# Kernel optimization log

Measured on AMD Instinct MI355X. Metric: run time of the kernel, lower is better.

Reference implementation:

```python
import jax, jax.numpy as jnp
import numpy as np

N, E, D, ED, H = 50000, 640000, 128, 64, 128
EPS = 1e-5


def _bn(x, gamma, beta):
    # BatchNorm1d in training mode: batch stats over rows, biased variance
    mean = jnp.mean(x, axis=0)
    var = jnp.mean(jnp.square(x - mean), axis=0)
    return (x - mean) * jax.lax.rsqrt(var + EPS) * gamma + beta


def setup_inputs() -> dict:
    key = jax.random.key(0)
    ks = jax.random.split(key, 12)

    def lin(k, fan_in, fan_out):
        return jax.random.normal(k, (fan_in, fan_out), jnp.float32) / np.sqrt(fan_in)

    return {
        "h": jax.random.normal(ks[0], (N, D), jnp.float32),
        "edge_attr": jax.random.normal(ks[1], (E, ED), jnp.float32),
        # msg MLP: Linear(2D+ED->H), BN(H), ReLU, Linear(H->H)
        "W1": lin(ks[2], 2 * D + ED, H), "b1": jnp.zeros((H,), jnp.float32),
        "g1": jnp.ones((H,), jnp.float32), "be1": jnp.zeros((H,), jnp.float32),
        "W2": lin(ks[3], H, H), "b2": jnp.zeros((H,), jnp.float32),
        # upd MLP: Linear(D+H->H), BN(H), ReLU, Linear(H->D)
        "W3": lin(ks[4], D + H, H), "b3": jnp.zeros((H,), jnp.float32),
        "g2": jnp.ones((H,), jnp.float32), "be2": jnp.zeros((H,), jnp.float32),
        "W4": lin(ks[5], H, D), "b4": jnp.zeros((D,), jnp.float32),
        # residual LayerNorm
        "ln_g": jnp.ones((D,), jnp.float32), "ln_b": jnp.zeros((D,), jnp.float32),
        "edge_index": jax.random.randint(ks[6], (2, E), 0, N, jnp.int32),
        "num_nodes": N,
    }


def reference(h, edge_attr, W1, b1, g1, be1, W2, b2, W3, b3, g2, be2, W4, b4,
              ln_g, ln_b, edge_index, num_nodes):
    src, dst = edge_index[0], edge_index[1]
    # messages: MLP_msg(h_src || h_dst || e)  -> [E, H]
    msg_in = jnp.concatenate([h[src], h[dst], edge_attr], axis=-1)  # [E, 2D+ED]
    x = _bn(msg_in @ W1 + b1, g1, be1)
    messages = jax.nn.relu(x) @ W2 + b2
    # scatter-sum aggregate into dst nodes -> [N, H]
    agg = jax.ops.segment_sum(messages, dst, num_segments=num_nodes)
    # update: MLP_upd(h || agg) -> [N, D]
    u = jnp.concatenate([h, agg], axis=-1)
    y = _bn(u @ W3 + b3, g2, be2)
    h_new = jax.nn.relu(y) @ W4 + b4
    # residual + LayerNorm
    z = h + h_new
    mu = jnp.mean(z, axis=-1, keepdims=True)
    var = jnp.mean(jnp.square(z - mu), axis=-1, keepdims=True)
    return (z - mu) * jax.lax.rsqrt(var + EPS) * ln_g + ln_b
```

## Files before the change

kernel.cpp:

```cpp
#include <hip/hip_runtime.h>
#include <hip/hip_bf16.h>

#define EPS 1e-5f
#define DIMH 128
#define K1 320
#define K3 256

typedef __attribute__((ext_vector_type(8))) short bf16x8;
typedef __attribute__((ext_vector_type(4))) short bf16x4;
typedef __attribute__((ext_vector_type(4))) float f32x4;

#define MFMA(a, b, c) __builtin_amdgcn_mfma_f32_16x16x32_bf16(a, b, c, 0, 0, 0)

static __device__ __forceinline__ unsigned short f2bf(float f) {
    union { float f; unsigned u; } v; v.f = f;
    unsigned r = v.u + 0x7FFF + ((v.u >> 16) & 1);
    return (unsigned short)(r >> 16);
}

__global__ void k_prep_w(const float* __restrict__ W1, const float* __restrict__ W3,
                         const float* __restrict__ W4,
                         unsigned short* __restrict__ W1t, unsigned short* __restrict__ W3c,
                         unsigned short* __restrict__ W4t) {
    int t = blockIdx.x * 256 + threadIdx.x;
    if (t < K1 * 128) { int k = t / 128, n = t % 128; W1t[n * K1 + k] = f2bf(W1[t]); }
    if (t < 128 * 128) {
        int k = t / 128, n = t % 128;
        W4t[n * 128 + k] = f2bf(W4[t]);
        W3c[n * K3 + k] = f2bf(W3[t]);
    }
}

__global__ void k_hb(const float* __restrict__ h, unsigned short* __restrict__ hb, int total8) {
    int t = blockIdx.x * 256 + threadIdx.x;
    if (t < total8) {
        float4 a = *(const float4*)(h + (size_t)t * 8);
        float4 b = *(const float4*)(h + (size_t)t * 8 + 4);
        union { bf16x8 v; unsigned short s[8]; } u;
        u.s[0] = f2bf(a.x); u.s[1] = f2bf(a.y); u.s[2] = f2bf(a.z); u.s[3] = f2bf(a.w);
        u.s[4] = f2bf(b.x); u.s[5] = f2bf(b.y); u.s[6] = f2bf(b.z); u.s[7] = f2bf(b.w);
        *(bf16x8*)(hb + (size_t)t * 8) = u.v;
    }
}

__global__ void k_w23(const float* __restrict__ W2, const float* __restrict__ W3,
                      unsigned short* __restrict__ W3c) {
    int t = blockIdx.x * 256 + threadIdx.x;
    int j = t & 127, i = t >> 7;
    float s = 0.f;
    for (int k = 0; k < 128; ++k) s += W2[i * 128 + k] * W3[(128 + k) * 128 + j];
    W3c[j * K3 + 128 + i] = f2bf(s);
}

__global__ void k_cvec(const float* __restrict__ b2, const float* __restrict__ W3,
                       float* __restrict__ cvec) {
    int j = threadIdx.x;
    float s = 0.f;
    for (int k = 0; k < 128; ++k) s += b2[k] * W3[(128 + k) * 128 + j];
    cvec[j] = s;
}

__global__ void k_bn(const float* __restrict__ stats, const float* __restrict__ g,
                     const float* __restrict__ be, float* __restrict__ st, float cnt) {
    int c = threadIdx.x;
    float mean = stats[c] / cnt;
    float var = stats[128 + c] / cnt - mean * mean;
    float s = g[c] * rsqrtf(var + EPS);
    st[c] = s;
    st[128 + c] = be[c] - mean * s;
}

__global__ void k_deg(const int* __restrict__ dst, int* __restrict__ deg, int E) {
    int e = blockIdx.x * 256 + threadIdx.x;
    if (e < E) atomicAdd(&deg[dst[e]], 1);
}

__global__ void k_scan(const int* __restrict__ deg, int* __restrict__ offs,
                       int* __restrict__ cursor, int NN) {
    __shared__ int ps[1024];
    int t = threadIdx.x;
    int chunk = (NN + 1023) >> 10;
    int c0 = t * chunk;
    int s = 0;
    for (int i = 0; i < chunk; ++i) { int id = c0 + i; if (id < NN) s += deg[id]; }
    ps[t] = s; __syncthreads();
    for (int off = 1; off < 1024; off <<= 1) {
        int v = (t >= off) ? ps[t - off] : 0;
        __syncthreads();
        ps[t] += v;
        __syncthreads();
    }
    int run = t ? ps[t - 1] : 0;
    for (int i = 0; i < chunk; ++i) {
        int id = c0 + i;
        if (id < NN) { cursor[id] = run; run += deg[id]; offs[id] = run; }
    }
}

__global__ void k_scatter(const int* __restrict__ dst, int* __restrict__ cursor,
                          int* __restrict__ elist, int E) {
    int e = blockIdx.x * 256 + threadIdx.x;
    if (e < E) {
        int pos = atomicAdd(&cursor[dst[e]], 1);
        elist[pos] = e;
    }
}

__global__ __launch_bounds__(256, 4) void k_msg1(
    const unsigned short* __restrict__ hb, const float* __restrict__ ea,
    const int* __restrict__ src, const int* __restrict__ dst,
    const unsigned short* __restrict__ W1t, const float* __restrict__ b1,
    unsigned short* __restrict__ xout, float* __restrict__ stats) {
    __shared__ unsigned short A[64 * K1];
    int tid = threadIdx.x, lane = tid & 63, w = tid >> 6;
    long e0 = (long)blockIdx.x * 64;

    bf16x8 bfr[10][2];
    {
        int n = (w << 5) + (lane & 15), kb = (lane >> 4) << 3;
#pragma unroll
        for (int nt = 0; nt < 2; ++nt) {
            const unsigned short* p = W1t + (size_t)(n + nt * 16) * K1 + kb;
#pragma unroll
            for (int ks = 0; ks < 10; ++ks) bfr[ks][nt] = *(const bf16x8*)(p + ks * 32);
        }
    }
    {
        int c16 = tid & 15, r2 = tid >> 4;
#pragma unroll
        for (int rr = 0; rr < 4; ++rr) {
            int row = rr * 16 + r2;
            long e = e0 + row;
            int s = src[e], d = dst[e];
            bf16x8 vs = *(const bf16x8*)(hb + (size_t)s * DIMH + c16 * 8);
            bf16x8 vd = *(const bf16x8*)(hb + (size_t)d * DIMH + c16 * 8);
            float4 ve = *(const float4*)(ea + (size_t)e * 64 + c16 * 4);
            int base = row * K1, sw = (row & 7) << 3;
            *(bf16x8*)&A[(base + c16 * 8) ^ sw] = vs;
            *(bf16x8*)&A[(base + 128 + c16 * 8) ^ sw] = vd;
            union { bf16x4 v4; unsigned short s4[4]; } u;
            u.s4[0] = f2bf(ve.x); u.s4[1] = f2bf(ve.y); u.s4[2] = f2bf(ve.z); u.s4[3] = f2bf(ve.w);
            *(bf16x4*)&A[(base + 256 + c16 * 4) ^ sw] = u.v4;
        }
    }
    __syncthreads();

    f32x4 acc[4][2] = {};
#pragma unroll
    for (int rg = 0; rg < 4; ++rg) {
        int arow = rg * 16 + (lane & 15);
        int base = arow * K1, sw = (arow & 7) << 3, kb = (lane >> 4) << 3;
#pragma unroll
        for (int ks = 0; ks < 10; ++ks) {
            bf16x8 af = *(const bf16x8*)&A[(base + ks * 32 + kb) ^ sw];
            acc[rg][0] = MFMA(af, bfr[ks][0], acc[rg][0]);
            acc[rg][1] = MFMA(af, bfr[ks][1], acc[rg][1]);
        }
    }
    int c0 = (w << 5) + (lane & 15);
    float bias0 = b1[c0], bias1 = b1[c0 + 16];
    float ss[2] = {0.f, 0.f}, sq[2] = {0.f, 0.f};
#pragma unroll
    for (int rg = 0; rg < 4; ++rg)
#pragma unroll
        for (int r = 0; r < 4; ++r) {
            long row = e0 + rg * 16 + ((lane >> 4) << 2) + r;
            float v0 = acc[rg][0][r] + bias0;
            float v1 = acc[rg][1][r] + bias1;
            ss[0] += v0; sq[0] += v0 * v0;
            ss[1] += v1; sq[1] += v1 * v1;
            xout[(size_t)row * DIMH + c0] = f2bf(v0);
            xout[(size_t)row * DIMH + c0 + 16] = f2bf(v1);
        }
#pragma unroll
    for (int nt = 0; nt < 2; ++nt) {
        ss[nt] += __shfl_xor(ss[nt], 16); ss[nt] += __shfl_xor(ss[nt], 32);
        sq[nt] += __shfl_xor(sq[nt], 16); sq[nt] += __shfl_xor(sq[nt], 32);
    }
    if (lane < 16) {
        atomicAdd(&stats[c0], ss[0]);        atomicAdd(&stats[c0 + 16], ss[1]);
        atomicAdd(&stats[128 + c0], sq[0]);  atomicAdd(&stats[128 + c0 + 16], sq[1]);
    }
}

__global__ __launch_bounds__(256, 8) void k_agg(
    const unsigned short* __restrict__ x, const float* __restrict__ st,
    const int* __restrict__ offs, const int* __restrict__ deg,
    const int* __restrict__ elist, float* __restrict__ R, int NN) {
    int lane = threadIdx.x & 63, w = threadIdx.x >> 6;
    int n = blockIdx.x * 4 + w;
    if (n >= NN) return;
    int c = lane * 2;
    float s0 = st[c], s1 = st[c + 1], t0 = st[128 + c], t1 = st[128 + c + 1];
    int end = offs[n], start = end - deg[n];
    float a0 = 0.f, a1 = 0.f;
    int i = start;
    for (; i + 1 < end; i += 2) {
        int e0 = elist[i], e1 = elist[i + 1];
        unsigned v0 = *(const unsigned*)(x + (size_t)e0 * DIMH + c);
        unsigned v1 = *(const unsigned*)(x + (size_t)e1 * DIMH + c);
        float f;
        f = __uint_as_float(v0 << 16) * s0 + t0;         a0 += fmaxf(f, 0.f);
        f = __uint_as_float(v0 & 0xffff0000u) * s1 + t1; a1 += fmaxf(f, 0.f);
        f = __uint_as_float(v1 << 16) * s0 + t0;         a0 += fmaxf(f, 0.f);
        f = __uint_as_float(v1 & 0xffff0000u) * s1 + t1; a1 += fmaxf(f, 0.f);
    }
    if (i < end) {
        int e0 = elist[i];
        unsigned v0 = *(const unsigned*)(x + (size_t)e0 * DIMH + c);
        float f;
        f = __uint_as_float(v0 << 16) * s0 + t0;         a0 += fmaxf(f, 0.f);
        f = __uint_as_float(v0 & 0xffff0000u) * s1 + t1; a1 += fmaxf(f, 0.f);
    }
    *(float2*)(R + (size_t)n * DIMH + c) = make_float2(a0, a1);
}

__global__ __launch_bounds__(256, 4) void k_upd1(
    const unsigned short* __restrict__ hb, const float* __restrict__ R,
    const unsigned short* __restrict__ W3c, const float* __restrict__ b3,
    const int* __restrict__ deg, const float* __restrict__ cvec,
    unsigned short* __restrict__ ypre, float* __restrict__ stats, int NN) {
    __shared__ unsigned short A[64 * K3];
    int tid = threadIdx.x, lane = tid & 63, w = tid >> 6;
    int n0 = blockIdx.x * 64;

    bf16x8 bfr[8][2];
    {
        int n = (w << 5) + (lane & 15), kb = (lane >> 4) << 3;
#pragma unroll
        for (int nt = 0; nt < 2; ++nt) {
            const unsigned short* p = W3c + (size_t)(n + nt * 16) * K3 + kb;
#pragma unroll
            for (int ks = 0; ks < 8; ++ks) bfr[ks][nt] = *(const bf16x8*)(p + ks * 32);
        }
    }
    {
        int c16 = tid & 15, r2 = tid >> 4;
#pragma unroll
        for (int rr = 0; rr < 4; ++rr) {
            int row = rr * 16 + r2;
            int node = n0 + row;
            bf16x8 vh = {};
            union { bf16x8 v8; unsigned short s8[8]; } ur;
            if (node < NN) {
                vh = *(const bf16x8*)(hb + (size_t)node * DIMH + c16 * 8);
                float4 r0 = *(const float4*)(R + (size_t)node * DIMH + c16 * 8);
                float4 r1 = *(const float4*)(R + (size_t)node * DIMH + c16 * 8 + 4);
                ur.s8[0] = f2bf(r0.x); ur.s8[1] = f2bf(r0.y); ur.s8[2] = f2bf(r0.z); ur.s8[3] = f2bf(r0.w);
                ur.s8[4] = f2bf(r1.x); ur.s8[5] = f2bf(r1.y); ur.s8[6] = f2bf(r1.z); ur.s8[7] = f2bf(r1.w);
            } else {
#pragma unroll
                for (int j = 0; j < 8; ++j) ur.s8[j] = 0;
            }
            int base = row * K3, sw = (row & 7) << 3;
            *(bf16x8*)&A[(base + c16 * 8) ^ sw] = vh;
            *(bf16x8*)&A[(base + 128 + c16 * 8) ^ sw] = ur.v8;
        }
    }
    __syncthreads();

    f32x4 acc[4][2] = {};
#pragma unroll
    for (int rg = 0; rg < 4; ++rg) {
        int arow = rg * 16 + (lane & 15);
        int base = arow * K3, sw = (arow & 7) << 3, kb = (lane >> 4) << 3;
#pragma unroll
        for (int ks = 0; ks < 8; ++ks) {
            bf16x8 af = *(const bf16x8*)&A[(base + ks * 32 + kb) ^ sw];
            acc[rg][0] = MFMA(af, bfr[ks][0], acc[rg][0]);
            acc[rg][1] = MFMA(af, bfr[ks][1], acc[rg][1]);
        }
    }
    int c0 = (w << 5) + (lane & 15);
    float bias0 = b3[c0], bias1 = b3[c0 + 16];
    float cv0 = cvec[c0], cv1 = cvec[c0 + 16];
    float ss[2] = {0.f, 0.f}, sq[2] = {0.f, 0.f};
#pragma unroll
    for (int rg = 0; rg < 4; ++rg)
#pragma unroll
        for (int r = 0; r < 4; ++r) {
            int node = n0 + rg * 16 + ((lane >> 4) << 2) + r;
            if (node < NN) {
                float dg = (float)deg[node];
                float v0 = acc[rg][0][r] + bias0 + dg * cv0;
                float v1 = acc[rg][1][r] + bias1 + dg * cv1;
                ss[0] += v0; sq[0] += v0 * v0;
                ss[1] += v1; sq[1] += v1 * v1;
                ypre[(size_t)node * DIMH + c0] = f2bf(v0);
                ypre[(size_t)node * DIMH + c0 + 16] = f2bf(v1);
            }
        }
#pragma unroll
    for (int nt = 0; nt < 2; ++nt) {
        ss[nt] += __shfl_xor(ss[nt], 16); ss[nt] += __shfl_xor(ss[nt], 32);
        sq[nt] += __shfl_xor(sq[nt], 16); sq[nt] += __shfl_xor(sq[nt], 32);
    }
    if (lane < 16) {
        atomicAdd(&stats[c0], ss[0]);        atomicAdd(&stats[c0 + 16], ss[1]);
        atomicAdd(&stats[128 + c0], sq[0]);  atomicAdd(&stats[128 + c0 + 16], sq[1]);
    }
}

__global__ __launch_bounds__(256, 2) void k_upd2(
    const unsigned short* __restrict__ ypre, const unsigned short* __restrict__ W4t,
    const float* __restrict__ b4, const float* __restrict__ st,
    const float* __restrict__ h, const float* __restrict__ lng,
    const float* __restrict__ lnb, float* __restrict__ out, int NN) {
    const int LDA = 136;
    __shared__ unsigned short A[64 * 136];
    __shared__ float sS[128], sT[128];
    __shared__ float rsum[64], rsq[64];
    int tid = threadIdx.x, lane = tid & 63, w = tid >> 6;
    int n0 = blockIdx.x * 64;
    if (tid < 128) { sS[tid] = st[tid]; sT[tid] = st[128 + tid]; }
    if (tid < 64) { rsum[tid] = 0.f; rsq[tid] = 0.f; }

    bf16x8 bfr[4][2];
    {
        int n = (w << 5) + (lane & 15), kb = (lane >> 4) << 3;
#pragma unroll
        for (int nt = 0; nt < 2; ++nt) {
            const unsigned short* p = W4t + (size_t)(n + nt * 16) * 128 + kb;
#pragma unroll
            for (int ks = 0; ks < 4; ++ks) bfr[ks][nt] = *(const bf16x8*)(p + ks * 32);
        }
    }
    __syncthreads();
    {
        int c16 = tid & 15, r2 = tid >> 4;
#pragma unroll
        for (int rr = 0; rr < 4; ++rr) {
            int row = rr * 16 + r2;
            int node = n0 + row;
            union { bf16x8 v8; unsigned short s[8]; } u;
            if (node < NN) {
                bf16x8 v = *(const bf16x8*)(ypre + (size_t)node * DIMH + c16 * 8);
#pragma unroll
                for (int j = 0; j < 8; ++j) {
                    int c = c16 * 8 + j;
                    union { unsigned uu; float f; } cvt; cvt.uu = ((unsigned)(unsigned short)v[j]) << 16;
                    float f = cvt.f * sS[c] + sT[c];
                    u.s[j] = f2bf(fmaxf(f, 0.f));
                }
            } else {
#pragma unroll
                for (int j = 0; j < 8; ++j) u.s[j] = 0;
            }
            *(bf16x8*)&A[row * LDA + c16 * 8] = u.v8;
        }
    }
    __syncthreads();

    f32x4 acc[4][2] = {};
#pragma unroll
    for (int rg = 0; rg < 4; ++rg) {
        int ab = (rg * 16 + (lane & 15)) * LDA + ((lane >> 4) << 3);
#pragma unroll
        for (int ks = 0; ks < 4; ++ks) {
            bf16x8 af = *(const bf16x8*)&A[ab + ks * 32];
            acc[rg][0] = MFMA(af, bfr[ks][0], acc[rg][0]);
            acc[rg][1] = MFMA(af, bfr[ks][1], acc[rg][1]);
        }
    }
    int c0 = (w << 5) + (lane & 15);
    float bias0 = b4[c0], bias1 = b4[c0 + 16];
    float z[4][2][4];
#pragma unroll
    for (int rg = 0; rg < 4; ++rg)
#pragma unroll
        for (int r = 0; r < 4; ++r) {
            int node = n0 + rg * 16 + ((lane >> 4) << 2) + r;
            float h0 = 0.f, h1 = 0.f;
            if (node < NN) {
                h0 = h[(size_t)node * DIMH + c0];
                h1 = h[(size_t)node * DIMH + c0 + 16];
            }
            z[rg][0][r] = acc[rg][0][r] + bias0 + h0;
            z[rg][1][r] = acc[rg][1][r] + bias1 + h1;
        }
#pragma unroll
    for (int rg = 0; rg < 4; ++rg)
#pragma unroll
        for (int r = 0; r < 4; ++r) {
            float ps = z[rg][0][r] + z[rg][1][r];
            float pq = z[rg][0][r] * z[rg][0][r] + z[rg][1][r] * z[rg][1][r];
#pragma unroll
            for (int m = 1; m < 16; m <<= 1) { ps += __shfl_xor(ps, m); pq += __shfl_xor(pq, m); }
            if ((lane & 15) == 0) {
                int row = rg * 16 + ((lane >> 4) << 2) + r;
                atomicAdd(&rsum[row], ps);
                atomicAdd(&rsq[row], pq);
            }
        }
    __syncthreads();
#pragma unroll
    for (int rg = 0; rg < 4; ++rg)
#pragma unroll
        for (int r = 0; r < 4; ++r) {
            int row = rg * 16 + ((lane >> 4) << 2) + r;
            int node = n0 + row;
            if (node < NN) {
                float mean = rsum[row] * (1.f / 128.f);
                float var = rsq[row] * (1.f / 128.f) - mean * mean;
                float rs = rsqrtf(var + EPS);
                float g0 = lng[c0], g1 = lng[c0 + 16];
                float be0 = lnb[c0], be1 = lnb[c0 + 16];
                out[(size_t)node * DIMH + c0] = (z[rg][0][r] - mean) * rs * g0 + be0;
                out[(size_t)node * DIMH + c0 + 16] = (z[rg][1][r] - mean) * rs * g1 + be1;
            }
        }
}

extern "C" void kernel_launch(void* const* d_in, const int* in_sizes, int n_in,
                              void* d_out, int out_size, void* d_ws, size_t ws_size,
                              hipStream_t stream) {
    const float* h   = (const float*)d_in[0];
    const float* ea  = (const float*)d_in[1];
    const float* W1  = (const float*)d_in[2];
    const float* b1  = (const float*)d_in[3];
    const float* g1  = (const float*)d_in[4];
    const float* be1 = (const float*)d_in[5];
    const float* W2  = (const float*)d_in[6];
    const float* b2  = (const float*)d_in[7];
    const float* W3  = (const float*)d_in[8];
    const float* b3  = (const float*)d_in[9];
    const float* g2  = (const float*)d_in[10];
    const float* be2 = (const float*)d_in[11];
    const float* W4  = (const float*)d_in[12];
    const float* b4  = (const float*)d_in[13];
    const float* lng = (const float*)d_in[14];
    const float* lnb = (const float*)d_in[15];
    const int* eidx  = (const int*)d_in[16];
    int NN = in_sizes[0] / DIMH;
    int E  = in_sizes[16] / 2;
    const int* src = eidx;
    const int* dst = eidx + E;

    char* ws = (char*)d_ws;
    size_t o = 0;
    unsigned short* W1t = (unsigned short*)(ws + o); o += 81920;
    unsigned short* W3c = (unsigned short*)(ws + o); o += 65536;
    unsigned short* W4t = (unsigned short*)(ws + o); o += 32768;
    float* cvec   = (float*)(ws + o); o += 512;
    float* stats1 = (float*)(ws + o); o += 1024;
    float* st1    = (float*)(ws + o); o += 1024;
    float* stats2 = (float*)(ws + o); o += 1024;
    float* st2    = (float*)(ws + o); o += 1024;
    int* deg    = (int*)(ws + o); o += 200192;
    int* offs   = (int*)(ws + o); o += 200192;
    int* cursor = (int*)(ws + o); o += 200192;
    int* elist  = (int*)(ws + o); o += (size_t)E * 4;
    unsigned short* hb = (unsigned short*)(ws + o); o += (size_t)NN * DIMH * 2;
    float* R = (float*)(ws + o); o += (size_t)NN * DIMH * 4;
    unsigned short* x = (unsigned short*)(ws + o);
    unsigned short* ypre = x;

    hipMemsetAsync(stats1, 0, 1024, stream);
    hipMemsetAsync(stats2, 0, 1024, stream);
    hipMemsetAsync(deg, 0, (size_t)NN * 4, stream);

    k_prep_w<<<(K1 * 128 + 255) / 256, 256, 0, stream>>>(W1, W3, W4, W1t, W3c, W4t);
    k_hb<<<(NN * DIMH / 8 + 255) / 256, 256, 0, stream>>>(h, hb, NN * DIMH / 8);
    k_w23<<<64, 256, 0, stream>>>(W2, W3, W3c);
    k_cvec<<<1, 128, 0, stream>>>(b2, W3, cvec);
    k_deg<<<(E + 255) / 256, 256, 0, stream>>>(dst, deg, E);
    k_scan<<<1, 1024, 0, stream>>>(deg, offs, cursor, NN);
    k_scatter<<<(E + 255) / 256, 256, 0, stream>>>(dst, cursor, elist, E);

    k_msg1<<<E / 64, 256, 0, stream>>>(hb, ea, src, dst, W1t, b1, x, stats1);
    k_bn<<<1, 128, 0, stream>>>(stats1, g1, be1, st1, (float)E);
    k_agg<<<(NN + 3) / 4, 256, 0, stream>>>(x, st1, offs, deg, elist, R, NN);

    int nb = (NN + 63) / 64;
    k_upd1<<<nb, 256, 0, stream>>>(hb, R, W3c, b3, deg, cvec, ypre, stats2, NN);
    k_bn<<<1, 128, 0, stream>>>(stats2, g2, be2, st2, (float)NN);
    k_upd2<<<nb, 256, 0, stream>>>(ypre, W4t, b4, st2, h, lng, lnb, (float*)d_out, NN);
}
```

Baseline: 832.9 us.

## Use direct global-to-LDS loads for gathers, stage output through LDS, unroll aggregation

The message kernel now gathers the source and destination node rows straight into shared memory with global_load_lds, into split swizzled buffers, and converts edge attributes in 8-wide chunks. Its bf16 output tile is staged in LDS and written back with coalesced 16-byte stores instead of scattered 2-byte stores. The aggregation loop is unrolled to four edges so more gather loads are in flight. Launch bounds for the message and update kernels drop to 3 blocks per SM, which allows more registers per thread but may lower occupancy.

```diff
diff --git a/kernel.cpp b/kernel.cpp
--- a/kernel.cpp
+++ b/kernel.cpp
@@ -16,6 +16,12 @@
     union { float f; unsigned u; } v; v.f = f;
     unsigned r = v.u + 0x7FFF + ((v.u >> 16) & 1);
     return (unsigned short)(r >> 16);
+}
+
+static __device__ __forceinline__ void gload16(const void* g, void* l) {
+    __builtin_amdgcn_global_load_lds(
+        (const __attribute__((address_space(1))) unsigned int*)g,
+        (__attribute__((address_space(3))) unsigned int*)l, 16, 0, 0);
 }
 
 __global__ void k_prep_w(const float* __restrict__ W1, const float* __restrict__ W3,
@@ -106,18 +112,21 @@
     }
 }
 
-__global__ __launch_bounds__(256, 4) void k_msg1(
+__global__ __launch_bounds__(256, 3) void k_msg1(
     const unsigned short* __restrict__ hb, const float* __restrict__ ea,
     const int* __restrict__ src, const int* __restrict__ dst,
     const unsigned short* __restrict__ W1t, const float* __restrict__ b1,
     unsigned short* __restrict__ xout, float* __restrict__ stats) {
-    __shared__ unsigned short A[64 * K1];
+    __shared__ unsigned short As[64 * 128];
+    __shared__ unsigned short Ad[64 * 128];
+    __shared__ unsigned short Ae[64 * 64];
     int tid = threadIdx.x, lane = tid & 63, w = tid >> 6;
+    int l15 = lane & 15, kq = lane >> 4;
     long e0 = (long)blockIdx.x * 64;
 
     bf16x8 bfr[10][2];
     {
-        int n = (w << 5) + (lane & 15), kb = (lane >> 4) << 3;
+        int n = (w << 5) + l15, kb = kq << 3;
 #pragma unroll
         for (int nt = 0; nt < 2; ++nt) {
             const unsigned short* p = W1t + (size_t)(n + nt * 16) * K1 + kb;
@@ -126,21 +135,30 @@
         }
     }
     {
-        int c16 = tid & 15, r2 = tid >> 4;
-#pragma unroll
-        for (int rr = 0; rr < 4; ++rr) {
-            int row = rr * 16 + r2;
+#pragma unroll
+        for (int j = 0; j < 4; ++j) {
+            int r4 = (w << 4) + j * 4;
+            int row = r4 + kq;
+            int u = l15 ^ (row & 7);
             long e = e0 + row;
-            int s = src[e], d = dst[e];
-            bf16x8 vs = *(const bf16x8*)(hb + (size_t)s * DIMH + c16 * 8);
-            bf16x8 vd = *(const bf16x8*)(hb + (size_t)d * DIMH + c16 * 8);
-            float4 ve = *(const float4*)(ea + (size_t)e * 64 + c16 * 4);
-            int base = row * K1, sw = (row & 7) << 3;
-            *(bf16x8*)&A[(base + c16 * 8) ^ sw] = vs;
-            *(bf16x8*)&A[(base + 128 + c16 * 8) ^ sw] = vd;
-            union { bf16x4 v4; unsigned short s4[4]; } u;
-            u.s4[0] = f2bf(ve.x); u.s4[1] = f2bf(ve.y); u.s4[2] = f2bf(ve.z); u.s4[3] = f2bf(ve.w);
-            *(bf16x4*)&A[(base + 256 + c16 * 4) ^ sw] = u.v4;
+            int sI = src[e], dI = dst[e];
+            gload16(hb + (size_t)sI * 128 + u * 8, &As[r4 * 128]);
+            gload16(hb + (size_t)dI * 128 + u * 8, &Ad[r4 * 128]);
+        }
+    }
+    {
+        int s8 = lane & 7, rq8 = lane >> 3;
+#pragma unroll
+        for (int p = 0; p < 2; ++p) {
+            int row = (w << 4) + p * 8 + rq8;
+            int u = (s8 ^ (row & 7)) << 3;
+            const float* ep = ea + (size_t)(e0 + row) * 64 + u;
+            float4 va = *(const float4*)ep;
+            float4 vb = *(const float4*)(ep + 4);
+            union { bf16x8 v; unsigned short s[8]; } uu;
+            uu.s[0] = f2bf(va.x); uu.s[1] = f2bf(va.y); uu.s[2] = f2bf(va.z); uu.s[3] = f2bf(va.w);
+            uu.s[4] = f2bf(vb.x); uu.s[5] = f2bf(vb.y); uu.s[6] = f2bf(vb.z); uu.s[7] = f2bf(vb.w);
+            *(bf16x8*)&Ae[row * 64 + s8 * 8] = uu.v;
         }
     }
     __syncthreads();
@@ -148,38 +166,60 @@
     f32x4 acc[4][2] = {};
 #pragma unroll
     for (int rg = 0; rg < 4; ++rg) {
-        int arow = rg * 16 + (lane & 15);
-        int base = arow * K1, sw = (arow & 7) << 3, kb = (lane >> 4) << 3;
-#pragma unroll
-        for (int ks = 0; ks < 10; ++ks) {
-            bf16x8 af = *(const bf16x8*)&A[(base + ks * 32 + kb) ^ sw];
+        int a = rg * 16 + l15;
+        int swz = a & 7;
+        const unsigned short* pAs = As + a * 128;
+        const unsigned short* pAd = Ad + a * 128;
+        const unsigned short* pAe = Ae + a * 64;
+#pragma unroll
+        for (int ks = 0; ks < 4; ++ks) {
+            bf16x8 af = *(const bf16x8*)(pAs + (((ks << 2) + kq) ^ swz) * 8);
             acc[rg][0] = MFMA(af, bfr[ks][0], acc[rg][0]);
             acc[rg][1] = MFMA(af, bfr[ks][1], acc[rg][1]);
         }
-    }
-    int c0 = (w << 5) + (lane & 15);
+#pragma unroll
+        for (int ks = 0; ks < 4; ++ks) {
+            bf16x8 af = *(const bf16x8*)(pAd + (((ks << 2) + kq) ^ swz) * 8);
+            acc[rg][0] = MFMA(af, bfr[4 + ks][0], acc[rg][0]);
+            acc[rg][1] = MFMA(af, bfr[4 + ks][1], acc[rg][1]);
+        }
+#pragma unroll
+        for (int ks = 0; ks < 2; ++ks) {
+            bf16x8 af = *(const bf16x8*)(pAe + (((ks << 2) + kq) ^ swz) * 8);
+            acc[rg][0] = MFMA(af, bfr[8 + ks][0], acc[rg][0]);
+            acc[rg][1] = MFMA(af, bfr[8 + ks][1], acc[rg][1]);
+        }
+    }
+    __syncthreads();
+    unsigned short* xt = As;
+    int c0 = (w << 5) + l15;
     float bias0 = b1[c0], bias1 = b1[c0 + 16];
-    float ss[2] = {0.f, 0.f}, sq[2] = {0.f, 0.f};
+    float ss0 = 0.f, ss1 = 0.f, sq0 = 0.f, sq1 = 0.f;
 #pragma unroll
     for (int rg = 0; rg < 4; ++rg)
 #pragma unroll
         for (int r = 0; r < 4; ++r) {
-            long row = e0 + rg * 16 + ((lane >> 4) << 2) + r;
+            int row = rg * 16 + (kq << 2) + r;
             float v0 = acc[rg][0][r] + bias0;
             float v1 = acc[rg][1][r] + bias1;
-            ss[0] += v0; sq[0] += v0 * v0;
-            ss[1] += v1; sq[1] += v1 * v1;
-            xout[(size_t)row * DIMH + c0] = f2bf(v0);
-            xout[(size_t)row * DIMH + c0 + 16] = f2bf(v1);
-        }
-#pragma unroll
-    for (int nt = 0; nt < 2; ++nt) {
-        ss[nt] += __shfl_xor(ss[nt], 16); ss[nt] += __shfl_xor(ss[nt], 32);
-        sq[nt] += __shfl_xor(sq[nt], 16); sq[nt] += __shfl_xor(sq[nt], 32);
-    }
+            ss0 += v0; sq0 += v0 * v0;
+            ss1 += v1; sq1 += v1 * v1;
+            xt[row * 128 + c0] = f2bf(v0);
+            xt[row * 128 + c0 + 16] = f2bf(v1);
+        }
+    __syncthreads();
+#pragma unroll
+    for (int p = 0; p < 4; ++p) {
+        int off8 = p * 2048 + tid * 8;
+        *(bf16x8*)(xout + (size_t)e0 * 128 + off8) = *(const bf16x8*)(xt + off8);
+    }
+    ss0 += __shfl_xor(ss0, 16); ss0 += __shfl_xor(ss0, 32);
+    sq0 += __shfl_xor(sq0, 16); sq0 += __shfl_xor(sq0, 32);
+    ss1 += __shfl_xor(ss1, 16); ss1 += __shfl_xor(ss1, 32);
+    sq1 += __shfl_xor(sq1, 16); sq1 += __shfl_xor(sq1, 32);
     if (lane < 16) {
-        atomicAdd(&stats[c0], ss[0]);        atomicAdd(&stats[c0 + 16], ss[1]);
-        atomicAdd(&stats[128 + c0], sq[0]);  atomicAdd(&stats[128 + c0 + 16], sq[1]);
+        atomicAdd(&stats[c0], ss0);        atomicAdd(&stats[c0 + 16], ss1);
+        atomicAdd(&stats[128 + c0], sq0);  atomicAdd(&stats[128 + c0 + 16], sq1);
     }
 }
 
@@ -192,30 +232,33 @@
     if (n >= NN) return;
     int c = lane * 2;
     float s0 = st[c], s1 = st[c + 1], t0 = st[128 + c], t1 = st[128 + c + 1];
-    int end = offs[n], start = end - deg[n];
+    int end = offs[n], i = end - deg[n];
     float a0 = 0.f, a1 = 0.f;
-    int i = start;
-    for (; i + 1 < end; i += 2) {
-        int e0 = elist[i], e1 = elist[i + 1];
+    for (; i + 3 < end; i += 4) {
+        int e0 = elist[i], e1 = elist[i + 1], e2 = elist[i + 2], e3 = elist[i + 3];
         unsigned v0 = *(const unsigned*)(x + (size_t)e0 * DIMH + c);
         unsigned v1 = *(const unsigned*)(x + (size_t)e1 * DIMH + c);
-        float f;
-        f = __uint_as_float(v0 << 16) * s0 + t0;         a0 += fmaxf(f, 0.f);
-        f = __uint_as_float(v0 & 0xffff0000u) * s1 + t1; a1 += fmaxf(f, 0.f);
-        f = __uint_as_float(v1 << 16) * s0 + t0;         a0 += fmaxf(f, 0.f);
-        f = __uint_as_float(v1 & 0xffff0000u) * s1 + t1; a1 += fmaxf(f, 0.f);
-    }
-    if (i < end) {
+        unsigned v2 = *(const unsigned*)(x + (size_t)e2 * DIMH + c);
+        unsigned v3 = *(const unsigned*)(x + (size_t)e3 * DIMH + c);
+        a0 += fmaxf(__uint_as_float(v0 << 16) * s0 + t0, 0.f);
+        a1 += fmaxf(__uint_as_float(v0 & 0xffff0000u) * s1 + t1, 0.f);
+        a0 += fmaxf(__uint_as_float(v1 << 16) * s0 + t0, 0.f);
+        a1 += fmaxf(__uint_as_float(v1 & 0xffff0000u) * s1 + t1, 0.f);
+        a0 += fmaxf(__uint_as_float(v2 << 16) * s0 + t0, 0.f);
+        a1 += fmaxf(__uint_as_float(v2 & 0xffff0000u) * s1 + t1, 0.f);
+        a0 += fmaxf(__uint_as_float(v3 << 16) * s0 + t0, 0.f);
+        a1 += fmaxf(__uint_as_float(v3 & 0xffff0000u) * s1 + t1, 0.f);
+    }
+    for (; i < end; ++i) {
         int e0 = elist[i];
         unsigned v0 = *(const unsigned*)(x + (size_t)e0 * DIMH + c);
-        float f;
-        f = __uint_as_float(v0 << 16) * s0 + t0;         a0 += fmaxf(f, 0.f);
-        f = __uint_as_float(v0 & 0xffff0000u) * s1 + t1; a1 += fmaxf(f, 0.f);
+        a0 += fmaxf(__uint_as_float(v0 << 16) * s0 + t0, 0.f);
+        a1 += fmaxf(__uint_as_float(v0 & 0xffff0000u) * s1 + t1, 0.f);
     }
     *(float2*)(R + (size_t)n * DIMH + c) = make_float2(a0, a1);
 }
 
-__global__ __launch_bounds__(256, 4) void k_upd1(
+__global__ __launch_bounds__(256, 3) void k_upd1(
     const unsigned short* __restrict__ hb, const float* __restrict__ R,
     const unsigned short* __restrict__ W3c, const float* __restrict__ b3,
     const int* __restrict__ deg, const float* __restrict__ cvec,
```

Measured after the change: 812.6 us. 1.02x faster.
